# Optimization experiments

Hardware: AMD Instinct MI355X
Metric: run time of the kernel (lower is better)

## Reference

```python
import jax, jax.numpy as jnp
import numpy as np

N = 100_000      # nodes
E = 1_600_000    # edges
D = 128          # dim_in == dim_h
L = 3            # num_layers
G = 512          # num graphs in batch
EPS = 1e-5       # BatchNorm1d eps


def setup_inputs() -> dict:
    key = jax.random.key(0)
    k1, k2, k3, k4 = jax.random.split(key, 4)
    x = jax.random.normal(k1, (N, D), dtype=jnp.float32)
    edge_index = jax.random.randint(k2, (2, E), 0, N, dtype=jnp.int64)
    batch = jnp.sort(jax.random.randint(k3, (N,), 0, G, dtype=jnp.int64))
    Ws = jax.random.normal(k4, (L, D, D), dtype=jnp.float32) * 0.05
    bs = jnp.zeros((L, D), dtype=jnp.float32)
    gammas = jnp.ones((L, D), dtype=jnp.float32)
    betas = jnp.zeros((L, D), dtype=jnp.float32)
    return {"x": x, "edge_index": edge_index, "batch": batch,
            "Ws": Ws, "bs": bs, "gammas": gammas, "betas": betas}


def reference(x, edge_index, batch, Ws, bs, gammas, betas):
    src, dst = edge_index[0], edge_index[1]
    # GCN symmetric normalization with self-loops (PyG GCNConv default):
    # deg counts incoming edges at dst, +1 for the self-loop.
    deg = jnp.zeros((N,), dtype=x.dtype).at[dst].add(1.0) + 1.0
    inv_sqrt = jax.lax.rsqrt(deg)
    edge_coeff = inv_sqrt[src] * inv_sqrt[dst]   # [E]
    self_coeff = inv_sqrt * inv_sqrt             # [N] self-loop weight deg^-1

    h = x
    for i in range(L):
        hw = h @ Ws[i]                                           # [N, D]
        agg = (jnp.zeros_like(hw).at[dst].add(hw[src] * edge_coeff[:, None])
               + hw * self_coeff[:, None] + bs[i])               # [N, D]
        # BatchNorm1d (training-mode batch statistics, biased variance)
        mean = agg.mean(axis=0)
        var = agg.var(axis=0)
        hn = (agg - mean) * jax.lax.rsqrt(var + EPS) * gammas[i] + betas[i]
        h = jax.nn.relu(hn)

    # global_add_pool: scatter-add node features by graph id
    return jax.ops.segment_sum(h, batch, num_segments=G)        # [G, D]
```

## Files before the change

kernel.cpp:

```cpp
#include <hip/hip_runtime.h>

#define D 128
#define CHUNK 512
#define NSLICE 8
#define SLW 16
#define ECAP 1024

using short8 = __attribute__((ext_vector_type(8))) short;
using f32x4  = __attribute__((ext_vector_type(4))) float;
using f32x2  = __attribute__((ext_vector_type(2))) float;
using u32x2  = __attribute__((ext_vector_type(2))) unsigned;

__device__ __forceinline__ unsigned short f2bf(float f){
  unsigned u = __builtin_bit_cast(unsigned, f);
  u += 0x7fffu + ((u >> 16) & 1u);
  return (unsigned short)(u >> 16);
}
__device__ __forceinline__ float bflo2f(unsigned v){
  return __builtin_bit_cast(float, v << 16);
}
__device__ __forceinline__ float bfhi2f(unsigned v){
  return __builtin_bit_cast(float, v & 0xffff0000u);
}
__device__ __forceinline__ float bfs2f(unsigned short v){
  return __builtin_bit_cast(float, ((unsigned)v) << 16);
}
__device__ __forceinline__ unsigned cvtpk(float lo, float hi){
  unsigned r;
  asm("v_cvt_pk_bf16_f32 %0, %1, %2" : "=v"(r) : "v"(lo), "v"(hi));
  return r;
}

__global__ void k_deg(const int* __restrict__ dst, int* __restrict__ deg,
                      int* __restrict__ rank, int E){
  int e = blockIdx.x * 256 + threadIdx.x;
  if (e < E) rank[e] = atomicAdd(&deg[dst[e]], 1);
}

__global__ void k_chunksum(const int* __restrict__ deg, int* __restrict__ csum, int n){
  __shared__ int s[256];
  int tid = threadIdx.x;
  int n0 = blockIdx.x * CHUNK + tid * 2;
  int v = 0;
  if (n0     < n) v += deg[n0];
  if (n0 + 1 < n) v += deg[n0 + 1];
  s[tid] = v; __syncthreads();
  for (int off = 128; off > 0; off >>= 1){
    if (tid < off) s[tid] += s[tid + off];
    __syncthreads();
  }
  if (tid == 0) csum[blockIdx.x] = s[0];
}

__global__ void k_scanchunks(int* __restrict__ csum, int nchunks){
  __shared__ int s[256];
  int tid = threadIdx.x;
  int v = (tid < nchunks) ? csum[tid] : 0;
  s[tid] = v; __syncthreads();
  for (int off = 1; off < 256; off <<= 1){
    int t = (tid >= off) ? s[tid - off] : 0;
    __syncthreads();
    s[tid] += t;
    __syncthreads();
  }
  if (tid < nchunks) csum[tid] = s[tid] - v;
}

__global__ void k_offsets(const int* __restrict__ deg, const int* __restrict__ csum,
                          int* __restrict__ offs, float* __restrict__ inv, int n){
  __shared__ int s[256];
  int tid = threadIdx.x;
  int n0 = blockIdx.x * CHUNK + tid * 2;
  int d0 = (n0     < n) ? deg[n0]     : 0;
  int d1 = (n0 + 1 < n) ? deg[n0 + 1] : 0;
  int pair = d0 + d1;
  s[tid] = pair; __syncthreads();
  for (int off = 1; off < 256; off <<= 1){
    int t = (tid >= off) ? s[tid - off] : 0;
    __syncthreads();
    s[tid] += t;
    __syncthreads();
  }
  int excl = s[tid] - pair + csum[blockIdx.x];
  if (n0     <= n) offs[n0]     = excl;
  if (n0 + 1 <= n) offs[n0 + 1] = excl + d0;
  if (n0     < n) inv[n0]     = rsqrtf((float)(d0 + 1));
  if (n0 + 1 < n) inv[n0 + 1] = rsqrtf((float)(d1 + 1));
}

__global__ __launch_bounds__(256)
void k_csrfill(const int* __restrict__ src, const int* __restrict__ dst,
               const int* __restrict__ offs, const int* __restrict__ rank,
               int* __restrict__ csrc, int E, int n){
  int part = blockIdx.x & 7;
  int blk  = blockIdx.x >> 3;
  int nblk = gridDim.x >> 3;
  int per = (n + 7) / 8;
  int d0 = part * per, d1 = min(d0 + per, n);
  int stride = nblk * 256;
  for (int e = blk * 256 + threadIdx.x; e < E; e += stride){
    int d = dst[e];
    if (d >= d0 && d < d1){
      csrc[offs[d] + rank[e]] = src[e];
    }
  }
}

#define WSTRIDE 136
__global__ __launch_bounds__(512)
void k_gemm(const float* __restrict__ hf, const unsigned short* __restrict__ hb,
            const float* __restrict__ W, const float* __restrict__ inv,
            const float* __restrict__ stats, const float* __restrict__ gamma,
            const float* __restrict__ beta, float invn,
            int do_norm, unsigned short* __restrict__ hwS, int nrows){
  __shared__ unsigned short Wt[128 * WSTRIDE];
  __shared__ float s_sc[128], s_sh[128];
  int tid = threadIdx.x;
  if (do_norm && tid < 128){
    float mean = stats[tid] * invn;
    float var = stats[128 + tid] * invn - mean * mean;
    float isd = rsqrtf(var + 1e-5f);
    float sc = gamma[tid] * isd;
    s_sc[tid] = sc;
    s_sh[tid] = beta[tid] - mean * sc;
  }
  for (int i = tid; i < 128 * 128; i += 512){
    int k = i >> 7, c = i & 127;
    Wt[c * WSTRIDE + k] = f2bf(W[i]);
  }
  __syncthreads();

  int wave = tid >> 6, lane = tid & 63;
  int r0 = blockIdx.x * 128 + wave * 16;
  int row = r0 + (lane & 15);
  int kg = lane >> 4;
  int rowc = row < nrows ? row : nrows - 1;

  short8 a[4];
  if (do_norm){
#pragma unroll
    for (int kt = 0; kt < 4; ++kt){
      int k0 = kt * 32 + kg * 8;
      int sl = k0 >> 4, o = k0 & 15;
      short8 raw = *(const short8*)(hb + ((long)sl * nrows + rowc) * SLW + o);
      unsigned u[4];
#pragma unroll
      for (int j = 0; j < 4; ++j){
        float lo = bfs2f((unsigned short)raw[2*j]);
        float hi = bfs2f((unsigned short)raw[2*j+1]);
        lo = fmaxf(0.f, lo * s_sc[k0+2*j]   + s_sh[k0+2*j]);
        hi = fmaxf(0.f, hi * s_sc[k0+2*j+1] + s_sh[k0+2*j+1]);
        u[j] = cvtpk(lo, hi);
      }
      a[kt] = *(short8*)u;
    }
  } else {
    const float* hrow = hf + (long)rowc * D;
#pragma unroll
    for (int kt = 0; kt < 4; ++kt){
      int k0 = kt * 32 + kg * 8;
      f32x4 v0 = *(const f32x4*)(hrow + k0);
      f32x4 v1 = *(const f32x4*)(hrow + k0 + 4);
      unsigned u[4];
      u[0] = cvtpk(v0[0], v0[1]);
      u[1] = cvtpk(v0[2], v0[3]);
      u[2] = cvtpk(v1[0], v1[1]);
      u[3] = cvtpk(v1[2], v1[3]);
      a[kt] = *(short8*)u;
    }
  }

  f32x4 acc[8] = {};
#pragma unroll
  for (int ct = 0; ct < 8; ++ct){
    int col = ct * 16 + (lane & 15);
    const unsigned short* bp = &Wt[col * WSTRIDE + kg * 8];
#pragma unroll
    for (int kt = 0; kt < 4; ++kt){
      short8 b = *(const short8*)(bp + kt * 32);
      acc[ct] = __builtin_amdgcn_mfma_f32_16x16x32_bf16(a[kt], b, acc[ct], 0, 0, 0);
    }
  }

  int colbase = lane & 15;
  int rowo = r0 + kg * 4;
  float ivr[4];
#pragma unroll
  for (int r = 0; r < 4; ++r) ivr[r] = inv[min(rowo + r, nrows - 1)];
#pragma unroll
  for (int ct = 0; ct < 8; ++ct){
#pragma unroll
    for (int r = 0; r < 4; ++r){
      int rr = rowo + r;
      if (rr < nrows)
        hwS[((long)ct * nrows + rr) * SLW + colbase] = f2bf(acc[ct][r] * ivr[r]);
    }
  }
}

__global__ __launch_bounds__(256)
void k_agg(const unsigned short* __restrict__ hwS, const float* __restrict__ inv,
           const int* __restrict__ offs, const int* __restrict__ csrc,
           const float* __restrict__ bias,
           unsigned* __restrict__ aggS, float* __restrict__ stats, int n,
           int ngroups){
  int g   = blockIdx.x & 7;
  int grp = blockIdx.x >> 3;
  int tid = threadIdx.x, lane = tid & 63, wv = tid >> 6;
  int ns = lane >> 2;
  int cp = lane & 3;
  int nwaves = ngroups * 4;
  int gw = grp * 4 + wv;
  int per = (n + nwaves - 1) / nwaves;
  int n0 = min(gw * per, n), n1 = min(n0 + per, n);

  const u32x2* slice2 = (const u32x2*)((const unsigned*)hwS + (long)g * n * 8);
  u32x2* oslice2 = (u32x2*)(aggS + (long)g * n * 8);

  __shared__ int stg[4][ECAP];

  int cb = g * 16 + cp * 4;
  float b0 = bias[cb], b1 = bias[cb + 1], b2 = bias[cb + 2], b3 = bias[cb + 3];
  float s0 = 0, s1 = 0, s2 = 0, s3 = 0;
  float q0 = 0, q1 = 0, q2 = 0, q3 = 0;

  for (int base = n0; base < n1; base += 16){
    int cend = min(base + 16, n1);
    int eBase = offs[base];
    int cnt = offs[cend] - eBase;
    int node = base + ns;
    bool act = node < n1;
    int ndc = act ? node : n1 - 1;
    int e  = offs[ndc];
    int ee = offs[ndc + 1];
    int rel = e - eBase;
    int len = ee - e;
    float a0 = 0, a1 = 0, a2 = 0, a3 = 0;

    if (cnt <= ECAP){
      for (int t = lane; t < cnt; t += 64) stg[wv][t] = csrc[eBase + t];
      int cm1 = cnt - 1;
      int p = 0;
      while (__any(p < len)){
        int i0 = stg[wv][min(rel + p,     cm1)];
        int i1 = stg[wv][min(rel + p + 1, cm1)];
        int i2 = stg[wv][min(rel + p + 2, cm1)];
        int i3 = stg[wv][min(rel + p + 3, cm1)];
        u32x2 v0 = slice2[(long)i0 * 4 + cp];
        u32x2 v1 = slice2[(long)i1 * 4 + cp];
        u32x2 v2 = slice2[(long)i2 * 4 + cp];
        u32x2 v3 = slice2[(long)i3 * 4 + cp];
        bool k0 = p < len, k1 = p + 1 < len, k2 = p + 2 < len, k3 = p + 3 < len;
        v0[0] = k0 ? v0[0] : 0u; v0[1] = k0 ? v0[1] : 0u;
        v1[0] = k1 ? v1[0] : 0u; v1[1] = k1 ? v1[1] : 0u;
        v2[0] = k2 ? v2[0] : 0u; v2[1] = k2 ? v2[1] : 0u;
        v3[0] = k3 ? v3[0] : 0u; v3[1] = k3 ? v3[1] : 0u;
        a0 += (bflo2f(v0[0]) + bflo2f(v1[0])) + (bflo2f(v2[0]) + bflo2f(v3[0]));
        a1 += (bfhi2f(v0[0]) + bfhi2f(v1[0])) + (bfhi2f(v2[0]) + bfhi2f(v3[0]));
        a2 += (bflo2f(v0[1]) + bflo2f(v1[1])) + (bflo2f(v2[1]) + bflo2f(v3[1]));
        a3 += (bfhi2f(v0[1]) + bfhi2f(v1[1])) + (bfhi2f(v2[1]) + bfhi2f(v3[1]));
        p += 4;
      }
    } else {
      int cm1 = cnt - 1;
      int p = 0;
      while (__any(p < len)){
        int i0 = csrc[eBase + min(rel + p,     cm1)];
        int i1 = csrc[eBase + min(rel + p + 1, cm1)];
        int i2 = csrc[eBase + min(rel + p + 2, cm1)];
        int i3 = csrc[eBase + min(rel + p + 3, cm1)];
        u32x2 v0 = slice2[(long)i0 * 4 + cp];
        u32x2 v1 = slice2[(long)i1 * 4 + cp];
        u32x2 v2 = slice2[(long)i2 * 4 + cp];
        u32x2 v3 = slice2[(long)i3 * 4 + cp];
        bool k0 = p < len, k1 = p + 1 < len, k2 = p + 2 < len, k3 = p + 3 < len;
        v0[0] = k0 ? v0[0] : 0u; v0[1] = k0 ? v0[1] : 0u;
        v1[0] = k1 ? v1[0] : 0u; v1[1] = k1 ? v1[1] : 0u;
        v2[0] = k2 ? v2[0] : 0u; v2[1] = k2 ? v2[1] : 0u;
        v3[0] = k3 ? v3[0] : 0u; v3[1] = k3 ? v3[1] : 0u;
        a0 += (bflo2f(v0[0]) + bflo2f(v1[0])) + (bflo2f(v2[0]) + bflo2f(v3[0]));
        a1 += (bfhi2f(v0[0]) + bfhi2f(v1[0])) + (bfhi2f(v2[0]) + bfhi2f(v3[0]));
        a2 += (bflo2f(v0[1]) + bflo2f(v1[1])) + (bflo2f(v2[1]) + bflo2f(v3[1]));
        a3 += (bfhi2f(v0[1]) + bfhi2f(v1[1])) + (bfhi2f(v2[1]) + bfhi2f(v3[1]));
        p += 4;
      }
    }

    if (act){
      u32x2 sv = slice2[(long)node * 4 + cp];
      float ivd = inv[node];
      a0 = (a0 + bflo2f(sv[0])) * ivd + b0;
      a1 = (a1 + bfhi2f(sv[0])) * ivd + b1;
      a2 = (a2 + bflo2f(sv[1])) * ivd + b2;
      a3 = (a3 + bfhi2f(sv[1])) * ivd + b3;
      u32x2 pk;
      pk[0] = ((unsigned)f2bf(a1) << 16) | (unsigned)f2bf(a0);
      pk[1] = ((unsigned)f2bf(a3) << 16) | (unsigned)f2bf(a2);
      __builtin_nontemporal_store(pk, oslice2 + (long)node * 4 + cp);
      s0 += a0; s1 += a1; s2 += a2; s3 += a3;
      q0 += a0 * a0; q1 += a1 * a1; q2 += a2 * a2; q3 += a3 * a3;
    }
  }

#pragma unroll
  for (int off = 4; off <= 32; off <<= 1){
    s0 += __shfl_xor(s0, off, 64); s1 += __shfl_xor(s1, off, 64);
    s2 += __shfl_xor(s2, off, 64); s3 += __shfl_xor(s3, off, 64);
    q0 += __shfl_xor(q0, off, 64); q1 += __shfl_xor(q1, off, 64);
    q2 += __shfl_xor(q2, off, 64); q3 += __shfl_xor(q3, off, 64);
  }

  __shared__ float red[4][4][8];
  if (ns == 0){
    red[wv][cp][0] = s0; red[wv][cp][1] = s1;
    red[wv][cp][2] = s2; red[wv][cp][3] = s3;
    red[wv][cp][4] = q0; red[wv][cp][5] = q1;
    red[wv][cp][6] = q2; red[wv][cp][7] = q3;
  }
  __syncthreads();
  if (tid < 4){
    float t[8] = {0,0,0,0,0,0,0,0};
#pragma unroll
    for (int w = 0; w < 4; ++w)
#pragma unroll
      for (int j = 0; j < 8; ++j) t[j] += red[w][tid][j];
    int c = g * 16 + tid * 4;
#pragma unroll
    for (int j = 0; j < 4; ++j){
      atomicAdd(&stats[c + j],       t[j]);
      atomicAdd(&stats[128 + c + j], t[4 + j]);
    }
  }
}

__global__ __launch_bounds__(256)
void k_pool(const unsigned* __restrict__ aggS, const float* __restrict__ stats,
            const float* __restrict__ gamma, const float* __restrict__ beta,
            float invn, const int* __restrict__ batch,
            float* __restrict__ out, int n){
  __shared__ float psc[128], psh[128];
  int tid = threadIdx.x, lane = tid & 63, wv = tid >> 6;
  if (tid < 128){
    float mean = stats[tid] * invn;
    float var = stats[128 + tid] * invn - mean * mean;
    float isd = rsqrtf(var + 1e-5f);
    float sc = gamma[tid] * isd;
    psc[tid] = sc;
    psh[tid] = beta[tid] - mean * sc;
  }
  __syncthreads();
  int gw = blockIdx.x * 4 + wv;
  int n0 = gw * 64;
  if (n0 >= n) return;
  int n1 = min(n0 + 64, n);
  int c0 = lane * 2;
  int sl = lane >> 3, cp = lane & 7;
  long sbase = (long)sl * n * 8;
  float sc0 = psc[c0], sc1 = psc[c0 + 1];
  float sh0 = psh[c0], sh1 = psh[c0 + 1];
  int g = batch[n0];
  float a0 = 0, a1 = 0;
  for (int nd = n0; nd < n1; ++nd){
    int gn = batch[nd];
    if (gn != g){
      atomicAdd(&out[(long)g * D + c0],     a0);
      atomicAdd(&out[(long)g * D + c0 + 1], a1);
      a0 = 0; a1 = 0; g = gn;
    }
    unsigned v = aggS[sbase + (long)nd * 8 + cp];
    a0 += fmaxf(0.f, bflo2f(v) * sc0 + sh0);
    a1 += fmaxf(0.f, bfhi2f(v) * sc1 + sh1);
  }
  atomicAdd(&out[(long)g * D + c0],     a0);
  atomicAdd(&out[(long)g * D + c0 + 1], a1);
}

extern "C" void kernel_launch(void* const* d_in, const int* in_sizes, int n_in,
                              void* d_out, int out_size, void* d_ws, size_t ws_size,
                              hipStream_t stream){
  const float* x      = (const float*)d_in[0];
  const int*   ei     = (const int*)d_in[1];
  const int*   batch  = (const int*)d_in[2];
  const float* Ws     = (const float*)d_in[3];
  const float* bs     = (const float*)d_in[4];
  const float* gammas = (const float*)d_in[5];
  const float* betas  = (const float*)d_in[6];

  const int E_ = in_sizes[1] / 2;
  const int N_ = in_sizes[2];
  const int* src = ei;
  const int* dst = ei + E_;

  char* p = (char*)d_ws;
  auto alloc = [&](size_t bytes) -> void* {
    void* r = (void*)p;
    p += (bytes + 255) & ~(size_t)255;
    return r;
  };
  unsigned*       bufA   = (unsigned*)      alloc((size_t)N_ * D * 2);
  unsigned short* hwS    = (unsigned short*)alloc((size_t)N_ * D * 2);
  int*            deg    = (int*)           alloc((size_t)N_ * 4);
  float*          inv    = (float*)         alloc((size_t)N_ * 4);
  int*            offs   = (int*)           alloc((size_t)(N_ + 1) * 4);
  int*            rank   = (int*)           alloc((size_t)E_ * 4);
  int*            csrc   = (int*)           alloc((size_t)E_ * 4);
  float*          stats  = (float*)         alloc(3 * 256 * 4);
  int*            csum   = (int*)           alloc(256 * 4);

  hipMemsetAsync(deg,    0, (size_t)N_ * 4, stream);
  hipMemsetAsync(stats,  0, 3 * 256 * 4, stream);
  hipMemsetAsync(d_out,  0, (size_t)out_size * 4, stream);

  float invn = 1.0f / (float)N_;
  int nchunks = (N_ + CHUNK - 1) / CHUNK;
  k_deg       <<<(E_ + 255) / 256, 256, 0, stream>>>(dst, deg, rank, E_);
  k_chunksum  <<<nchunks, 256, 0, stream>>>(deg, csum, N_);
  k_scanchunks<<<1, 256, 0, stream>>>(csum, nchunks);
  k_offsets   <<<nchunks, 256, 0, stream>>>(deg, csum, offs, inv, N_);
  k_csrfill   <<<2048, 256, 0, stream>>>(src, dst, offs, rank, csrc, E_, N_);

  int gemm_blocks = (N_ + 127) / 128;
  int ngroups = 256;
  for (int l = 0; l < 3; ++l){
    const float* st = (l == 0) ? stats : stats + (size_t)(l - 1) * 256;
    const float* gm = (l == 0) ? gammas : gammas + (size_t)(l - 1) * D;
    const float* bt = (l == 0) ? betas : betas + (size_t)(l - 1) * D;
    k_gemm<<<gemm_blocks, 512, 0, stream>>>(x, (const unsigned short*)bufA,
                                            Ws + (size_t)l * D * D, inv,
                                            st, gm, bt, invn,
                                            (l == 0) ? 0 : 1, hwS, N_);
    k_agg<<<ngroups * 8, 256, 0, stream>>>(hwS, inv, offs, csrc, bs + (size_t)l * D,
                                           bufA, stats + (size_t)l * 256, N_, ngroups);
  }
  k_pool<<<(N_ + 255) / 256, 256, 0, stream>>>(bufA, stats + 2 * 256,
                                               gammas + 2 * D, betas + 2 * D, invn,
                                               batch, (float*)d_out, N_);
}
```

Measured before the change: 543.3 us.

## Replace LDS edge staging with register-prefetched index loads in aggregation

The aggregation kernel no longer stages each 16-node chunk's source indices into shared memory. Each lane now reads csrc directly and prefetches the next four indices while gathering the current four feature rows, a software-pipelined index load. Dropping the 16 KB LDS array is meant to raise occupancy, and the grid is doubled to 512 groups to supply more waves. The cost is uncoalesced per-lane index loads in place of the cooperative staged load, plus more partial-stat accumulations.

```diff
diff --git a/kernel.cpp b/kernel.cpp
--- a/kernel.cpp
+++ b/kernel.cpp
@@ -4,7 +4,6 @@
 #define CHUNK 512
 #define NSLICE 8
 #define SLW 16
-#define ECAP 1024
 
 using short8 = __attribute__((ext_vector_type(8))) short;
 using f32x4  = __attribute__((ext_vector_type(4))) float;
@@ -217,73 +216,43 @@
   const u32x2* slice2 = (const u32x2*)((const unsigned*)hwS + (long)g * n * 8);
   u32x2* oslice2 = (u32x2*)(aggS + (long)g * n * 8);
 
-  __shared__ int stg[4][ECAP];
-
   int cb = g * 16 + cp * 4;
   float b0 = bias[cb], b1 = bias[cb + 1], b2 = bias[cb + 2], b3 = bias[cb + 3];
   float s0 = 0, s1 = 0, s2 = 0, s3 = 0;
   float q0 = 0, q1 = 0, q2 = 0, q3 = 0;
 
   for (int base = n0; base < n1; base += 16){
-    int cend = min(base + 16, n1);
-    int eBase = offs[base];
-    int cnt = offs[cend] - eBase;
     int node = base + ns;
     bool act = node < n1;
     int ndc = act ? node : n1 - 1;
     int e  = offs[ndc];
     int ee = offs[ndc + 1];
-    int rel = e - eBase;
-    int len = ee - e;
     float a0 = 0, a1 = 0, a2 = 0, a3 = 0;
 
-    if (cnt <= ECAP){
-      for (int t = lane; t < cnt; t += 64) stg[wv][t] = csrc[eBase + t];
-      int cm1 = cnt - 1;
-      int p = 0;
-      while (__any(p < len)){
-        int i0 = stg[wv][min(rel + p,     cm1)];
-        int i1 = stg[wv][min(rel + p + 1, cm1)];
-        int i2 = stg[wv][min(rel + p + 2, cm1)];
-        int i3 = stg[wv][min(rel + p + 3, cm1)];
-        u32x2 v0 = slice2[(long)i0 * 4 + cp];
-        u32x2 v1 = slice2[(long)i1 * 4 + cp];
-        u32x2 v2 = slice2[(long)i2 * 4 + cp];
-        u32x2 v3 = slice2[(long)i3 * 4 + cp];
-        bool k0 = p < len, k1 = p + 1 < len, k2 = p + 2 < len, k3 = p + 3 < len;
-        v0[0] = k0 ? v0[0] : 0u; v0[1] = k0 ? v0[1] : 0u;
-        v1[0] = k1 ? v1[0] : 0u; v1[1] = k1 ? v1[1] : 0u;
-        v2[0] = k2 ? v2[0] : 0u; v2[1] = k2 ? v2[1] : 0u;
-        v3[0] = k3 ? v3[0] : 0u; v3[1] = k3 ? v3[1] : 0u;
-        a0 += (bflo2f(v0[0]) + bflo2f(v1[0])) + (bflo2f(v2[0]) + bflo2f(v3[0]));
-        a1 += (bfhi2f(v0[0]) + bfhi2f(v1[0])) + (bfhi2f(v2[0]) + bfhi2f(v3[0]));
-        a2 += (bflo2f(v0[1]) + bflo2f(v1[1])) + (bflo2f(v2[1]) + bflo2f(v3[1]));
-        a3 += (bfhi2f(v0[1]) + bfhi2f(v1[1])) + (bfhi2f(v2[1]) + bfhi2f(v3[1]));
-        p += 4;
-      }
-    } else {
-      int cm1 = cnt - 1;
-      int p = 0;
-      while (__any(p < len)){
-        int i0 = csrc[eBase + min(rel + p,     cm1)];
-        int i1 = csrc[eBase + min(rel + p + 1, cm1)];
-        int i2 = csrc[eBase + min(rel + p + 2, cm1)];
-        int i3 = csrc[eBase + min(rel + p + 3, cm1)];
-        u32x2 v0 = slice2[(long)i0 * 4 + cp];
-        u32x2 v1 = slice2[(long)i1 * 4 + cp];
-        u32x2 v2 = slice2[(long)i2 * 4 + cp];
-        u32x2 v3 = slice2[(long)i3 * 4 + cp];
-        bool k0 = p < len, k1 = p + 1 < len, k2 = p + 2 < len, k3 = p + 3 < len;
-        v0[0] = k0 ? v0[0] : 0u; v0[1] = k0 ? v0[1] : 0u;
-        v1[0] = k1 ? v1[0] : 0u; v1[1] = k1 ? v1[1] : 0u;
-        v2[0] = k2 ? v2[0] : 0u; v2[1] = k2 ? v2[1] : 0u;
-        v3[0] = k3 ? v3[0] : 0u; v3[1] = k3 ? v3[1] : 0u;
-        a0 += (bflo2f(v0[0]) + bflo2f(v1[0])) + (bflo2f(v2[0]) + bflo2f(v3[0]));
-        a1 += (bfhi2f(v0[0]) + bfhi2f(v1[0])) + (bfhi2f(v2[0]) + bfhi2f(v3[0]));
-        a2 += (bflo2f(v0[1]) + bflo2f(v1[1])) + (bflo2f(v2[1]) + bflo2f(v3[1]));
-        a3 += (bfhi2f(v0[1]) + bfhi2f(v1[1])) + (bfhi2f(v2[1]) + bfhi2f(v3[1]));
-        p += 4;
-      }
+    int i0 = csrc[(e     < ee) ? e     : 0];
+    int i1 = csrc[(e + 1 < ee) ? e + 1 : 0];
+    int i2 = csrc[(e + 2 < ee) ? e + 2 : 0];
+    int i3 = csrc[(e + 3 < ee) ? e + 3 : 0];
+    while (__any(e < ee)){
+      int j0 = csrc[(e + 4 < ee) ? e + 4 : 0];
+      int j1 = csrc[(e + 5 < ee) ? e + 5 : 0];
+      int j2 = csrc[(e + 6 < ee) ? e + 6 : 0];
+      int j3 = csrc[(e + 7 < ee) ? e + 7 : 0];
+      u32x2 v0 = slice2[(long)i0 * 4 + cp];
+      u32x2 v1 = slice2[(long)i1 * 4 + cp];
+      u32x2 v2 = slice2[(long)i2 * 4 + cp];
+      u32x2 v3 = slice2[(long)i3 * 4 + cp];
+      bool k0 = e < ee, k1 = e + 1 < ee, k2 = e + 2 < ee, k3 = e + 3 < ee;
+      v0[0] = k0 ? v0[0] : 0u; v0[1] = k0 ? v0[1] : 0u;
+      v1[0] = k1 ? v1[0] : 0u; v1[1] = k1 ? v1[1] : 0u;
+      v2[0] = k2 ? v2[0] : 0u; v2[1] = k2 ? v2[1] : 0u;
+      v3[0] = k3 ? v3[0] : 0u; v3[1] = k3 ? v3[1] : 0u;
+      a0 += (bflo2f(v0[0]) + bflo2f(v1[0])) + (bflo2f(v2[0]) + bflo2f(v3[0]));
+      a1 += (bfhi2f(v0[0]) + bfhi2f(v1[0])) + (bfhi2f(v2[0]) + bfhi2f(v3[0]));
+      a2 += (bflo2f(v0[1]) + bflo2f(v1[1])) + (bflo2f(v2[1]) + bflo2f(v3[1]));
+      a3 += (bfhi2f(v0[1]) + bfhi2f(v1[1])) + (bfhi2f(v2[1]) + bfhi2f(v3[1]));
+      i0 = j0; i1 = j1; i2 = j2; i3 = j3;
+      e += 4;
     }
 
     if (act){
@@ -420,7 +389,7 @@
   k_csrfill   <<<2048, 256, 0, stream>>>(src, dst, offs, rank, csrc, E_, N_);
 
   int gemm_blocks = (N_ + 127) / 128;
-  int ngroups = 256;
+  int ngroups = 512;
   for (int l = 0; l < 3; ++l){
     const float* st = (l == 0) ? stats : stats + (size_t)(l - 1) * 256;
     const float* gm = (l == 0) ? gammas : gammas + (size_t)(l - 1) * D;
```

Result: faster. 519.7 us (-4.3%).
